# Performance work log

Measured on AMD Instinct MI355X. Metric: run time of the kernel, lower is better.

## Reference

```python
import jax, jax.numpy as jnp
import numpy as np
from jax import lax

EPS = 1e-07
B, NPRIM, NSEC, DP, DS = 512, 1152, 10, 8, 16


def setup_inputs() -> dict:
    key = jax.random.key(0)
    ks = jax.random.split(key, 12)
    inp = {}
    inp['x'] = jax.random.uniform(ks[0], (B, 28, 28, 1), dtype=jnp.float32)
    inp['labels'] = jax.random.randint(ks[1], (B,), 0, NSEC)
    # conv1: 9x9, 1 -> 256, relu ; conv2 (primary caps): 9x9 stride2, 256 -> 256
    inp['conv1_k'] = jax.random.normal(ks[2], (9, 9, 1, 256), dtype=jnp.float32) * 0.05
    inp['conv1_b'] = jnp.zeros((256,), dtype=jnp.float32)
    inp['conv2_k'] = jax.random.normal(ks[3], (9, 9, 256, 256), dtype=jnp.float32) * 0.02
    inp['conv2_b'] = jnp.zeros((256,), dtype=jnp.float32)
    # pose transform W: [1152, 10, 16, 8]
    inp['w'] = jax.random.normal(ks[4], (NPRIM, NSEC, DS, DP), dtype=jnp.float32) * 0.05
    # decoder
    inp['d1_w'] = jax.random.normal(ks[5], (NSEC * DS, 512), dtype=jnp.float32) * 0.05
    inp['d1_b'] = jnp.zeros((512,), dtype=jnp.float32)
    inp['d2_w'] = jax.random.normal(ks[6], (512, 1024), dtype=jnp.float32) * 0.05
    inp['d2_b'] = jnp.zeros((1024,), dtype=jnp.float32)
    inp['d3_w'] = jax.random.normal(ks[7], (1024, 784), dtype=jnp.float32) * 0.05
    inp['d3_b'] = jnp.zeros((784,), dtype=jnp.float32)
    return inp


def _conv(x, k, b, stride):
    y = lax.conv_general_dilated(x, k, (stride, stride), 'VALID',
                                 dimension_numbers=('NHWC', 'HWIO', 'NHWC'))
    return y + b


def _squash(s):
    # s: [..., D]
    s_norm = jnp.linalg.norm(s, axis=-1, keepdims=True)
    sq = jnp.square(s_norm)
    return sq / (1.0 + sq) * s / (s_norm + EPS)


def reference(x, labels, conv1_k, conv1_b, conv2_k, conv2_b, w,
              d1_w, d1_b, d2_w, d2_b, d3_w, d3_b):
    h = jax.nn.relu(_conv(x, conv1_k, conv1_b, 1))        # [B,20,20,256]
    p = _conv(h, conv2_k, conv2_b, 2)                      # [B,6,6,256]
    u = p.reshape(x.shape[0], NPRIM, DP)                   # [B,1152,8]
    # u_hat[b,n,s,d] = sum_p w[n,s,d,p] * u[b,n,p]
    u_hat = jnp.einsum('nsdp,bnp->bnsd', w, u)             # [B,1152,10,16]

    b_logits = jnp.zeros((x.shape[0], NPRIM, NSEC, 1), dtype=u_hat.dtype)
    v = None
    for _ in range(3):  # r routing iterations (fixed, small)
        c = jax.nn.softmax(b_logits, axis=-2)              # softmax over 10 secondary caps
        s = jnp.sum(c * u_hat, axis=1, keepdims=True)      # [B,1,10,16]
        v = _squash(s)                                     # [B,1,10,16]
        agreement = jnp.sum(u_hat * v, axis=-1, keepdims=True)  # [B,1152,10,1]
        b_logits = b_logits + agreement

    y = jax.nn.one_hot(labels, NSEC, dtype=v.dtype)        # [B,10]
    mask = y[:, None, :, None]                             # [B,1,10,1]
    v_masked = mask * v
    v_flat = v_masked.reshape(-1, NSEC * DS)               # [B,160]
    r1 = jax.nn.relu(v_flat @ d1_w + d1_b)
    r2 = jax.nn.relu(r1 @ d2_w + d2_b)
    recon = jax.nn.sigmoid(r2 @ d3_w + d3_b)               # [B,784]
    return v, recon
```

## Files before the change

### kernel.cpp

```cpp
#include <hip/hip_runtime.h>

#define USH unsigned short

__device__ inline float bf2f(USH u){ return __uint_as_float(((unsigned)u)<<16); }
__device__ inline USH f2bf(float f){
  unsigned u = __float_as_uint(f);
  return (USH)((u + 0x7FFFu + ((u>>16)&1u))>>16);
}

typedef __attribute__((ext_vector_type(8))) short bf16x8;
typedef __attribute__((ext_vector_type(4))) float f32x4;

__device__ inline void gll16(const USH* g, USH* l){
  __builtin_amdgcn_global_load_lds((const __attribute__((address_space(1))) void*)g,
                                   (__attribute__((address_space(3))) void*)l, 16, 0, 0);
}

__global__ __launch_bounds__(256) void im2col_k(
    const float* __restrict__ x, USH* __restrict__ xcol)
{
  int b = blockIdx.x, t = threadIdx.x;
  __shared__ float xs[784];
  for (int i = t; i < 784; i += 256) xs[i] = x[b*784 + i];
  __syncthreads();
  USH* dst = xcol + (size_t)b*38400;
  for (int idx = t; idx < 38400; idx += 256) {
    int sp = idx / 96, k = idx - sp*96;
    int y = sp / 20, xx = sp - y*20;
    USH v = 0;
    if (k < 81) {
      int dy = k / 9, dx = k - dy*9;
      v = f2bf(xs[(y+dy)*28 + xx + dx]);
    }
    dst[idx] = v;
  }
}

__global__ __launch_bounds__(256) void tr_k1(const float* __restrict__ k1, USH* __restrict__ k1T)
{
  int n = threadIdx.x;
  for (int k = 0; k < 96; ++k)
    k1T[n*96 + k] = (k < 81) ? f2bf(k1[k*256 + n]) : (USH)0;
}

__global__ __launch_bounds__(256) void gemm1(
    const USH* __restrict__ xcol, const USH* __restrict__ k1T,
    const float* __restrict__ b1, USH* __restrict__ h)
{
  int t = threadIdx.x;
  int m0 = blockIdx.x * 64;
  int lane = t & 63, wave = t >> 6;
  int wn = wave * 64;
  int fr = lane & 15, fq = lane >> 4;

  f32x4 acc[4][4];
#pragma unroll
  for (int i = 0; i < 4; ++i)
#pragma unroll
    for (int j = 0; j < 4; ++j)
#pragma unroll
      for (int r = 0; r < 4; ++r) acc[i][j][r] = 0.f;

#pragma unroll
  for (int kt = 0; kt < 3; ++kt) {
    int kc = kt*32 + fq*8;
    bf16x8 af[4], bg[4];
#pragma unroll
    for (int mf = 0; mf < 4; ++mf)
      af[mf] = *(const bf16x8*)&xcol[(size_t)(m0 + mf*16 + fr)*96 + kc];
#pragma unroll
    for (int nf = 0; nf < 4; ++nf)
      bg[nf] = *(const bf16x8*)&k1T[(size_t)(wn + nf*16 + fr)*96 + kc];
#pragma unroll
    for (int mf = 0; mf < 4; ++mf)
#pragma unroll
      for (int nf = 0; nf < 4; ++nf)
        acc[mf][nf] = __builtin_amdgcn_mfma_f32_16x16x32_bf16(af[mf], bg[nf], acc[mf][nf], 0,0,0);
  }

#pragma unroll
  for (int mf = 0; mf < 4; ++mf)
#pragma unroll
    for (int nf = 0; nf < 4; ++nf) {
      int n = wn + nf*16 + fr;
      float bias = b1[n];
#pragma unroll
      for (int r = 0; r < 4; ++r) {
        int m = m0 + mf*16 + fq*4 + r;
        float v = acc[mf][nf][r] + bias;
        h[(size_t)m*256 + n] = f2bf(v > 0.f ? v : 0.f);
      }
    }
}

__global__ __launch_bounds__(256) void tr_k2(const float* __restrict__ k2, USH* __restrict__ k2T)
{
  __shared__ float tile[32][33];
  int kb = blockIdx.x*32, nb = blockIdx.y*32;
  int tx = threadIdx.x & 31, ty = threadIdx.x >> 5;
#pragma unroll
  for (int r = 0; r < 4; ++r) {
    int k = kb + ty + r*8;
    tile[ty + r*8][tx] = k2[(size_t)k*256 + nb + tx];
  }
  __syncthreads();
#pragma unroll
  for (int r = 0; r < 4; ++r) {
    int n = nb + ty + r*8;
    k2T[(size_t)n*20736 + kb + tx] = f2bf(tile[tx][ty + r*8]);
  }
}

__global__ __launch_bounds__(256) void conv2_mfma(
    const USH* __restrict__ h, const USH* __restrict__ k2T,
    float* __restrict__ up)
{
  __shared__ __align__(16) USH Asm[2][128*64];
  __shared__ __align__(16) USH Bsm[2][64*64];
  int t = threadIdx.x;
  int mb = blockIdx.x, nb = blockIdx.y, ksl = blockIdx.z;

  int sg = (((t&7) ^ ((t>>3)&7)) << 3);

  int arow_off[4];
#pragma unroll
  for (int i = 0; i < 4; ++i) {
    int row = (t>>3) + i*32;
    int m = mb*128 + row;
    int bb = m/36, r = m - bb*36;
    int oy = r/6, ox = r - oy*6;
    arow_off[i] = bb*102400 + oy*10240 + ox*512 + sg;
  }
  int brow_off[2];
#pragma unroll
  for (int i = 0; i < 2; ++i) {
    int nl = (t>>3) + i*32;
    brow_off[i] = (nb*64 + nl)*20736 + sg;
  }

  int lane = t & 63;
  int wave = t >> 6;
  int wm = (wave>>1)*64, wn = (wave&1)*32;
  int fr = lane & 15, fq = lane >> 4;

  f32x4 acc[4][2];
#pragma unroll
  for (int i = 0; i < 4; ++i)
#pragma unroll
    for (int j = 0; j < 2; ++j)
#pragma unroll
      for (int r = 0; r < 4; ++r) acc[i][j][r] = 0.f;

  int rg0 = (((0*4 + fq) ^ (fr&7)) << 3);
  int rg1 = (((1*4 + fq) ^ (fr&7)) << 3);

#define STAGE(buf, kt) do {                                            \
    int j_ = (kt) >> 2;                                                \
    int cin0_ = ((kt) & 3) << 6;                                       \
    int dy_ = j_/9, dx_ = j_ - dy_*9;                                  \
    int koff_ = (dy_*20 + dx_)*256 + cin0_;                            \
    USH* Ad_ = &Asm[buf][(t>>6)*512];                                  \
    USH* Bd_ = &Bsm[buf][(t>>6)*512];                                  \
    _Pragma("unroll")                                                  \
    for (int i_ = 0; i_ < 4; ++i_) gll16(h + arow_off[i_] + koff_, Ad_ + i_*2048); \
    _Pragma("unroll")                                                  \
    for (int i_ = 0; i_ < 2; ++i_) gll16(k2T + brow_off[i_] + (kt)*64, Bd_ + i_*2048); \
  } while(0)

  const int k0 = ksl*81, kend = k0 + 81;
  STAGE(0, k0);
  __syncthreads();

  int cur = 0;
  for (int kt = k0; kt < kend; ++kt) {
    if (kt + 1 < kend) STAGE(cur^1, kt+1);

    bf16x8 af[4][2], bg[2][2];
#pragma unroll
    for (int mf = 0; mf < 4; ++mf) {
      af[mf][0] = *(const bf16x8*)&Asm[cur][(wm + mf*16 + fr)*64 + rg0];
      af[mf][1] = *(const bf16x8*)&Asm[cur][(wm + mf*16 + fr)*64 + rg1];
    }
#pragma unroll
    for (int nf = 0; nf < 2; ++nf) {
      bg[nf][0] = *(const bf16x8*)&Bsm[cur][(wn + nf*16 + fr)*64 + rg0];
      bg[nf][1] = *(const bf16x8*)&Bsm[cur][(wn + nf*16 + fr)*64 + rg1];
    }
#pragma unroll
    for (int mf = 0; mf < 4; ++mf)
#pragma unroll
      for (int nf = 0; nf < 2; ++nf) {
        acc[mf][nf] = __builtin_amdgcn_mfma_f32_16x16x32_bf16(af[mf][0], bg[nf][0], acc[mf][nf], 0,0,0);
        acc[mf][nf] = __builtin_amdgcn_mfma_f32_16x16x32_bf16(af[mf][1], bg[nf][1], acc[mf][nf], 0,0,0);
      }
    __syncthreads();
    cur ^= 1;
  }
#undef STAGE

  float* dst = up + (size_t)ksl*4718592;
#pragma unroll
  for (int mf = 0; mf < 4; ++mf)
#pragma unroll
    for (int nf = 0; nf < 2; ++nf) {
      int n = nb*64 + wn + nf*16 + fr;
#pragma unroll
      for (int r = 0; r < 4; ++r) {
        int m = mb*128 + wm + mf*16 + fq*4 + r;
        dst[(size_t)m*256 + n] = acc[mf][nf][r];
      }
    }
}

__global__ __launch_bounds__(256) void reduce_u(
    const float* __restrict__ up, const float* __restrict__ b2, float* __restrict__ u)
{
  int i = blockIdx.x*256 + threadIdx.x;
  f32x4 a = *(const f32x4*)&up[(size_t)i*4];
  f32x4 b = *(const f32x4*)&up[4718592ull + (size_t)i*4];
  f32x4 c = *(const f32x4*)&up[9437184ull + (size_t)i*4];
  f32x4 d = *(const f32x4*)&up[14155776ull + (size_t)i*4];
  int n0 = (i*4) & 255;
  f32x4 o;
#pragma unroll
  for (int j = 0; j < 4; ++j) o[j] = (a[j] + b[j]) + (c[j] + d[j]) + b2[n0 + j];
  *(f32x4*)&u[(size_t)i*4] = o;
}

__global__ __launch_bounds__(192) void wsum_tr(const float* __restrict__ w,
    float* __restrict__ Ws)
{
  int n = blockIdx.x, t = threadIdx.x;
  __shared__ float wn[1280];
  for (int i = t; i < 1280; i += 192) wn[i] = w[n*1280 + i];
  __syncthreads();
  if (t < 160) {
#pragma unroll
    for (int p = 0; p < 8; ++p)
      Ws[((size_t)n*8 + p)*160 + t] = wn[(t>>4)*128 + (t&15)*8 + p];
  }
}

__global__ __launch_bounds__(192) void p1gemm(const float* __restrict__ u,
    const float* __restrict__ Ws, float* __restrict__ part)
{
  int b0 = blockIdx.x*32, k0 = blockIdx.y*288;
  int t = threadIdx.x;
  __shared__ float usm[288*36];
  for (int i = t; i < 288*32; i += 192) {
    int bl = i/288, kk = i - bl*288;
    usm[kk*36 + bl] = u[(size_t)(b0+bl)*9216 + k0 + kk];
  }
  __syncthreads();
  if (t < 160) {
    const float* wp = Ws + (size_t)k0*160 + t;
#pragma unroll 1
    for (int half = 0; half < 2; ++half) {
      float acc[16];
#pragma unroll
      for (int i = 0; i < 16; ++i) acc[i] = 0.f;
      for (int kk = 0; kk < 288; ++kk) {
        float wv = wp[(size_t)kk*160];
        const f32x4* ub = (const f32x4*)&usm[kk*36 + half*16];
        f32x4 u0 = ub[0], u1 = ub[1], u2 = ub[2], u3 = ub[3];
#pragma unroll
        for (int i = 0; i < 4; ++i) {
          acc[i]    += u0[i]*wv;
          acc[4+i]  += u1[i]*wv;
          acc[8+i]  += u2[i]*wv;
          acc[12+i] += u3[i]*wv;
        }
      }
      float* pp = &part[((size_t)blockIdx.y*512 + b0 + half*16)*160 + t];
#pragma unroll
      for (int i = 0; i < 16; ++i) pp[(size_t)i*160] = acc[i];
    }
  }
}

__global__ __launch_bounds__(192) void squash1(const float* __restrict__ part,
    float* __restrict__ vout)
{
  int b = blockIdx.x, t = threadIdx.x;
  if (t < 160) {
    float sv = 0.f;
    for (int ks = 0; ks < 32; ++ks) sv += part[((size_t)ks*512 + b)*160 + t];
    sv *= 0.1f;
    float n2 = sv*sv;
    n2 += __shfl_xor(n2, 1, 16);
    n2 += __shfl_xor(n2, 2, 16);
    n2 += __shfl_xor(n2, 4, 16);
    n2 += __shfl_xor(n2, 8, 16);
    float nrm = sqrtf(n2);
    float o = (n2/(1.f + n2)) * sv / (nrm + 1e-7f);
    vout[b*160 + t] = o;
  }
}

__global__ __launch_bounds__(256) void uhat_kernel(
    const float* __restrict__ u, const float* __restrict__ w, USH* __restrict__ uh)
{
  int n = blockIdx.x, b0 = blockIdx.y*64;
  int t = threadIdx.x;
  __shared__ float wsm[20*65];
  __shared__ float usm[512];
  for (int i = t; i < 1280; i += 256) wsm[(i>>6)*65 + (i&63)] = w[n*1280 + i];
  for (int i = t; i < 512; i += 256) {
    int bl = i>>3, p = i&7;
    usm[i] = u[(size_t)(b0+bl)*9216 + n*8 + p];
  }
  __syncthreads();
  USH* dst = uh + ((size_t)n*512 + b0)*160;
  for (int v = t; v < 1280; v += 256) {
    int bl = v/20, oct = v - bl*20;
    const float* upt = &usm[bl*8];
    bf16x8 pk;
#pragma unroll
    for (int j = 0; j < 8; ++j) {
      const float* wp = &wsm[oct*65 + j*8];
      float a = 0.f;
#pragma unroll
      for (int p = 0; p < 8; ++p) a += wp[p]*upt[p];
      pk[j] = (short)f2bf(a);
    }
    *(bf16x8*)&dst[(size_t)v*8] = pk;
  }
}

template<int PASS>
__global__ __launch_bounds__(256) void route_part(
    const USH* __restrict__ uh, const float* __restrict__ vin,
    float* __restrict__ L, float* __restrict__ partR)
{
  int b = blockIdx.x, nc = blockIdx.y;
  int t = threadIdx.x;
  int lane = t & 63, w = t >> 6;
  int grp = lane >> 4, s = lane & 15;
  int stream = w*4 + grp;
  bool act = s < 10;

  float vr[16];
  {
    const float* vp = vin + b*160 + s*16;
#pragma unroll
    for (int d = 0; d < 16; ++d) vr[d] = act ? vp[d] : 0.f;
  }
  float acc[16];
#pragma unroll
  for (int d = 0; d < 16; ++d) acc[d] = 0.f;

  int nbase = nc*288 + stream*18;
  for (int ni = 0; ni < 18; ++ni) {
    int n = nbase + ni;
    float uv[16];
    if (act) {
      const USH* upt = uh + ((size_t)n*512 + b)*160 + s*16;
      bf16x8 p0 = *(const bf16x8*)upt;
      bf16x8 p1 = *(const bf16x8*)(upt + 8);
#pragma unroll
      for (int d = 0; d < 8; ++d) { uv[d] = bf2f((USH)p0[d]); uv[8+d] = bf2f((USH)p1[d]); }
    } else {
#pragma unroll
      for (int d = 0; d < 16; ++d) uv[d] = 0.f;
    }

    float dot = 0.f;
#pragma unroll
    for (int d = 0; d < 16; ++d) dot += uv[d]*vr[d];
    float lg;
    if (PASS == 2) {
      lg = dot;
      if (act) L[((size_t)n*512 + b)*10 + s] = dot;
    } else {
      lg = act ? (L[((size_t)n*512 + b)*10 + s] + dot) : 0.f;
    }
    if (!act) lg = -1e30f;
    float mx = lg;
    mx = fmaxf(mx, __shfl_xor(mx, 1, 16));
    mx = fmaxf(mx, __shfl_xor(mx, 2, 16));
    mx = fmaxf(mx, __shfl_xor(mx, 4, 16));
    mx = fmaxf(mx, __shfl_xor(mx, 8, 16));
    float e = __expf(lg - mx);
    float sum = e;
    sum += __shfl_xor(sum, 1, 16);
    sum += __shfl_xor(sum, 2, 16);
    sum += __shfl_xor(sum, 4, 16);
    sum += __shfl_xor(sum, 8, 16);
    float c = e / sum;
#pragma unroll
    for (int d = 0; d < 16; ++d) acc[d] += c*uv[d];
  }

  __shared__ float red[16][168];
  if (act) {
#pragma unroll
    for (int d = 0; d < 16; ++d) red[stream][s*16 + d] = acc[d];
  }
  __syncthreads();
  if (t < 160) {
    float sv = 0.f;
#pragma unroll
    for (int k = 0; k < 16; ++k) sv += red[k][t];
    partR[((size_t)nc*512 + b)*160 + t] = sv;
  }
}

template<int PASS>
__global__ __launch_bounds__(192) void squash_part(const float* __restrict__ partR,
    float* __restrict__ vout, float* __restrict__ vext)
{
  int b = blockIdx.x, t = threadIdx.x;
  if (t < 160) {
    float sv = 0.f;
#pragma unroll
    for (int nc = 0; nc < 4; ++nc) sv += partR[((size_t)nc*512 + b)*160 + t];
    float n2 = sv*sv;
    n2 += __shfl_xor(n2, 1, 16);
    n2 += __shfl_xor(n2, 2, 16);
    n2 += __shfl_xor(n2, 4, 16);
    n2 += __shfl_xor(n2, 8, 16);
    float nrm = sqrtf(n2);
    float o = (n2/(1.f + n2)) * sv / (nrm + 1e-7f);
    vout[b*160 + t] = o;
    if (PASS == 3) vext[b*160 + t] = o;
  }
}

__global__ __launch_bounds__(512) void d1_kernel(const float* __restrict__ v3,
    const int* __restrict__ labels, const float* __restrict__ w,
    const float* __restrict__ bias, float* __restrict__ r1)
{
  int b = blockIdx.x; int j = threadIdx.x;
  int lb = labels[b];
  float acc = bias[j];
#pragma unroll
  for (int d = 0; d < 16; ++d)
    acc += v3[b*160 + lb*16 + d] * w[(lb*16 + d)*512 + j];
  r1[(size_t)b*512 + j] = acc > 0.f ? acc : 0.f;
}

__global__ __launch_bounds__(256) void d2_kernel(const float* __restrict__ a,
    const float* __restrict__ w, const float* __restrict__ bias, float* __restrict__ o)
{
  int j = blockIdx.x*256 + threadIdx.x;
  int b0 = blockIdx.y*4;
  __shared__ float as[4*512];
  for (int i = threadIdx.x; i < 4*512; i += 256) as[i] = a[(size_t)(b0 + (i>>9))*512 + (i&511)];
  __syncthreads();
  float acc[4];
  float bs = bias[j];
#pragma unroll
  for (int i = 0; i < 4; ++i) acc[i] = bs;
  for (int k = 0; k < 512; ++k) {
    float wv = w[(size_t)k*1024 + j];
#pragma unroll
    for (int i = 0; i < 4; ++i) acc[i] += as[i*512 + k]*wv;
  }
#pragma unroll
  for (int i = 0; i < 4; ++i)
    o[(size_t)(b0+i)*1024 + j] = acc[i] > 0.f ? acc[i] : 0.f;
}

__global__ __launch_bounds__(256) void d3_kernel(const float* __restrict__ a,
    const float* __restrict__ w, const float* __restrict__ bias, float* __restrict__ o)
{
  int j = blockIdx.x*256 + threadIdx.x;
  int b0 = blockIdx.y*4;
  __shared__ float as[4*1024];
  for (int i = threadIdx.x; i < 4*1024; i += 256) as[i] = a[(size_t)(b0 + (i>>10))*1024 + (i&1023)];
  __syncthreads();
  if (j < 784) {
    float acc[4];
    float bs = bias[j];
#pragma unroll
    for (int i = 0; i < 4; ++i) acc[i] = bs;
    for (int k = 0; k < 1024; ++k) {
      float wv = w[(size_t)k*784 + j];
#pragma unroll
      for (int i = 0; i < 4; ++i) acc[i] += as[i*1024 + k]*wv;
    }
#pragma unroll
    for (int i = 0; i < 4; ++i)
      o[(size_t)(b0+i)*784 + j] = 1.f/(1.f + __expf(-acc[i]));
  }
}

extern "C" void kernel_launch(void* const* d_in, const int* in_sizes, int n_in,
                              void* d_out, int out_size, void* d_ws, size_t ws_size,
                              hipStream_t stream)
{
  const float* x   = (const float*)d_in[0];
  const int*   lab = (const int*)  d_in[1];
  const float* k1  = (const float*)d_in[2];
  const float* b1  = (const float*)d_in[3];
  const float* k2  = (const float*)d_in[4];
  const float* b2  = (const float*)d_in[5];
  const float* w   = (const float*)d_in[6];
  const float* d1w = (const float*)d_in[7];
  const float* d1b = (const float*)d_in[8];
  const float* d2w = (const float*)d_in[9];
  const float* d2b = (const float*)d_in[10];
  const float* d3w = (const float*)d_in[11];
  const float* d3b = (const float*)d_in[12];
  float* out = (float*)d_out;

  char* ws = (char*)d_ws;
  USH*   uh    = (USH*)(ws + 0);
  USH*   h     = (USH*)(ws + 0);
  float* up    = (float*)(ws + 104857600ull);
  USH*   xcol  = (USH*)(ws + 142606336ull);
  float* u     = (float*)(ws + 188743680ull);
  USH*   k2T   = (USH*)(ws + 207618048ull);
  float* part  = (float*)(ws + 207618048ull);
  float* partR = (float*)(ws + 207618048ull);
  float* L     = (float*)(ws + 218234880ull);
  float* Wsum  = (float*)(ws + 218234880ull);
  USH*   k1T   = (USH*)(ws + 241827840ull);
  float* v1    = (float*)(ws + 242155520ull);
  float* v2    = (float*)(ws + 242483200ull);
  float* v3    = (float*)(ws + 242810880ull);
  float* r1    = (float*)(ws + 243138560ull);
  float* r2    = (float*)(ws + 244187136ull);

  im2col_k<<<512, 256, 0, stream>>>(x, xcol);
  tr_k1<<<1, 256, 0, stream>>>(k1, k1T);
  gemm1<<<3200, 256, 0, stream>>>(xcol, k1T, b1, h);

  tr_k2<<<dim3(648,8), 256, 0, stream>>>(k2, k2T);
  conv2_mfma<<<dim3(144,4,4), 256, 0, stream>>>(h, k2T, up);
  reduce_u<<<4608, 256, 0, stream>>>(up, b2, u);

  wsum_tr<<<1152, 192, 0, stream>>>(w, Wsum);
  p1gemm<<<dim3(16,32), 192, 0, stream>>>(u, Wsum, part);
  squash1<<<512, 192, 0, stream>>>(part, v1);

  uhat_kernel<<<dim3(1152,8), 256, 0, stream>>>(u, w, uh);

  route_part<2><<<dim3(512,4), 256, 0, stream>>>(uh, v1, L, partR);
  squash_part<2><<<512, 192, 0, stream>>>(partR, v2, nullptr);
  route_part<3><<<dim3(512,4), 256, 0, stream>>>(uh, v2, L, partR);
  squash_part<3><<<512, 192, 0, stream>>>(partR, v3, out);

  d1_kernel<<<512, 512, 0, stream>>>(v3, lab, d1w, d1b, r1);
  d2_kernel<<<dim3(4,128), 256, 0, stream>>>(r1, d2w, d2b, r2);
  d3_kernel<<<dim3(4,128), 256, 0, stream>>>(r2, d3w, d3b, out + 81920);
}
```

Baseline: 689.1 us.

## Fuse u_hat computation into routing passes instead of materializing bf16 u_hat

Removes the separate uhat kernel that wrote a ~189MB bf16 u_hat tensor and instead recomputes u_hat on the fly inside each routing pass from u and W staged in LDS with double-buffered W tiles. Blocks are retiled to 16 primary capsules by 16 batch elements, giving 72 partial sums that the squash kernel now reduces. This trades the large global write and two full reads for extra FMAs and per-iteration barriers, and it also computes u_hat in fp32 rather than bf16.

Measured after the change: 731.5 us. 1.06x slower.

```diff
diff --git a/kernel.cpp b/kernel.cpp
--- a/kernel.cpp
+++ b/kernel.cpp
@@ -297,84 +297,75 @@
   }
 }
 
-__global__ __launch_bounds__(256) void uhat_kernel(
-    const float* __restrict__ u, const float* __restrict__ w, USH* __restrict__ uh)
-{
-  int n = blockIdx.x, b0 = blockIdx.y*64;
+template<int PASS>
+__global__ __launch_bounds__(256) void route_ns(
+    const float* __restrict__ u, const float* __restrict__ w,
+    const float* __restrict__ vin, float* __restrict__ L,
+    float* __restrict__ partR)
+{
+  int ng = blockIdx.x, bc = blockIdx.y;
+  int n0 = ng*16, b0 = bc*16;
   int t = threadIdx.x;
-  __shared__ float wsm[20*65];
-  __shared__ float usm[512];
-  for (int i = t; i < 1280; i += 256) wsm[(i>>6)*65 + (i&63)] = w[n*1280 + i];
-  for (int i = t; i < 512; i += 256) {
-    int bl = i>>3, p = i&7;
-    usm[i] = u[(size_t)(b0+bl)*9216 + n*8 + p];
-  }
-  __syncthreads();
-  USH* dst = uh + ((size_t)n*512 + b0)*160;
-  for (int v = t; v < 1280; v += 256) {
-    int bl = v/20, oct = v - bl*20;
-    const float* upt = &usm[bl*8];
-    bf16x8 pk;
-#pragma unroll
-    for (int j = 0; j < 8; ++j) {
-      const float* wp = &wsm[oct*65 + j*8];
-      float a = 0.f;
-#pragma unroll
-      for (int p = 0; p < 8; ++p) a += wp[p]*upt[p];
-      pk[j] = (short)f2bf(a);
-    }
-    *(bf16x8*)&dst[(size_t)v*8] = pk;
-  }
-}
-
-template<int PASS>
-__global__ __launch_bounds__(256) void route_part(
-    const USH* __restrict__ uh, const float* __restrict__ vin,
-    float* __restrict__ L, float* __restrict__ partR)
-{
-  int b = blockIdx.x, nc = blockIdx.y;
-  int t = threadIdx.x;
-  int lane = t & 63, w = t >> 6;
-  int grp = lane >> 4, s = lane & 15;
-  int stream = w*4 + grp;
+  int lane = t & 63;
+  int s = lane & 15;
+  int bl = (t >> 6)*4 + (lane >> 4);
   bool act = s < 10;
+  int sw = act ? s : 0;
+  int b = b0 + bl;
+
+  __shared__ float u_lds[16][132];
+  __shared__ __align__(16) float wsm[2][20*68];
+
+  for (int i = t; i < 16*128; i += 256) {
+    int b_ = i >> 7, off = i & 127;
+    u_lds[b_][off] = u[(size_t)(b0+b_)*9216 + n0*8 + off];
+  }
+  for (int i = t; i < 1280; i += 256)
+    wsm[0][(i>>6)*68 + (i&63)] = w[(size_t)n0*1280 + i];
 
   float vr[16];
   {
-    const float* vp = vin + b*160 + s*16;
-#pragma unroll
-    for (int d = 0; d < 16; ++d) vr[d] = act ? vp[d] : 0.f;
+    const float* vp = vin + (size_t)b*160 + sw*16;
+#pragma unroll
+    for (int d = 0; d < 16; ++d) vr[d] = vp[d];
   }
   float acc[16];
 #pragma unroll
   for (int d = 0; d < 16; ++d) acc[d] = 0.f;
 
-  int nbase = nc*288 + stream*18;
-  for (int ni = 0; ni < 18; ++ni) {
-    int n = nbase + ni;
-    float uv[16];
-    if (act) {
-      const USH* upt = uh + ((size_t)n*512 + b)*160 + s*16;
-      bf16x8 p0 = *(const bf16x8*)upt;
-      bf16x8 p1 = *(const bf16x8*)(upt + 8);
-#pragma unroll
-      for (int d = 0; d < 8; ++d) { uv[d] = bf2f((USH)p0[d]); uv[8+d] = bf2f((USH)p1[d]); }
-    } else {
-#pragma unroll
-      for (int d = 0; d < 16; ++d) uv[d] = 0.f;
+  __syncthreads();
+
+  int cur = 0;
+  for (int ni = 0; ni < 16; ++ni) {
+    int n = n0 + ni;
+    if (ni + 1 < 16)
+      for (int i = t; i < 1280; i += 256)
+        wsm[cur^1][(i>>6)*68 + (i&63)] = w[(size_t)(n+1)*1280 + i];
+
+    f32x4 u0 = *(const f32x4*)&u_lds[bl][ni*8];
+    f32x4 u1 = *(const f32x4*)&u_lds[bl][ni*8 + 4];
+
+    float uh[16];
+#pragma unroll
+    for (int d = 0; d < 16; ++d) {
+      const float* wr = &wsm[cur][(2*sw + (d>>3))*68 + (d&7)*8];
+      f32x4 wa = *(const f32x4*)wr;
+      f32x4 wb = *(const f32x4*)(wr + 4);
+      uh[d] = wa[0]*u0[0]+wa[1]*u0[1]+wa[2]*u0[2]+wa[3]*u0[3]
+            + wb[0]*u1[0]+wb[1]*u1[1]+wb[2]*u1[2]+wb[3]*u1[3];
     }
 
     float dot = 0.f;
 #pragma unroll
-    for (int d = 0; d < 16; ++d) dot += uv[d]*vr[d];
+    for (int d = 0; d < 16; ++d) dot += uh[d]*vr[d];
+
     float lg;
     if (PASS == 2) {
-      lg = dot;
+      lg = act ? dot : -1e30f;
       if (act) L[((size_t)n*512 + b)*10 + s] = dot;
     } else {
-      lg = act ? (L[((size_t)n*512 + b)*10 + s] + dot) : 0.f;
-    }
-    if (!act) lg = -1e30f;
+      lg = act ? (dot + L[((size_t)n*512 + b)*10 + s]) : -1e30f;
+    }
     float mx = lg;
     mx = fmaxf(mx, __shfl_xor(mx, 1, 16));
     mx = fmaxf(mx, __shfl_xor(mx, 2, 16));
@@ -388,32 +379,32 @@
     sum += __shfl_xor(sum, 8, 16);
     float c = e / sum;
 #pragma unroll
-    for (int d = 0; d < 16; ++d) acc[d] += c*uv[d];
-  }
-
-  __shared__ float red[16][168];
+    for (int d = 0; d < 16; ++d) acc[d] += c*uh[d];
+
+    __syncthreads();
+    cur ^= 1;
+  }
+
   if (act) {
-#pragma unroll
-    for (int d = 0; d < 16; ++d) red[stream][s*16 + d] = acc[d];
-  }
-  __syncthreads();
-  if (t < 160) {
-    float sv = 0.f;
-#pragma unroll
-    for (int k = 0; k < 16; ++k) sv += red[k][t];
-    partR[((size_t)nc*512 + b)*160 + t] = sv;
+    float* pp = &partR[((size_t)ng*512 + b)*160 + s*16];
+#pragma unroll
+    for (int q = 0; q < 4; ++q) {
+      f32x4 o;
+#pragma unroll
+      for (int j = 0; j < 4; ++j) o[j] = acc[q*4 + j];
+      *(f32x4*)(pp + q*4) = o;
+    }
   }
 }
 
 template<int PASS>
-__global__ __launch_bounds__(192) void squash_part(const float* __restrict__ partR,
+__global__ __launch_bounds__(192) void squash72(const float* __restrict__ partR,
     float* __restrict__ vout, float* __restrict__ vext)
 {
   int b = blockIdx.x, t = threadIdx.x;
   if (t < 160) {
     float sv = 0.f;
-#pragma unroll
-    for (int nc = 0; nc < 4; ++nc) sv += partR[((size_t)nc*512 + b)*160 + t];
+    for (int g = 0; g < 72; ++g) sv += partR[((size_t)g*512 + b)*160 + t];
     float n2 = sv*sv;
     n2 += __shfl_xor(n2, 1, 16);
     n2 += __shfl_xor(n2, 2, 16);
@@ -505,14 +496,13 @@
   float* out = (float*)d_out;
 
   char* ws = (char*)d_ws;
-  USH*   uh    = (USH*)(ws + 0);
   USH*   h     = (USH*)(ws + 0);
+  float* partR = (float*)(ws + 0);
   float* up    = (float*)(ws + 104857600ull);
   USH*   xcol  = (USH*)(ws + 142606336ull);
   float* u     = (float*)(ws + 188743680ull);
   USH*   k2T   = (USH*)(ws + 207618048ull);
   float* part  = (float*)(ws + 207618048ull);
-  float* partR = (float*)(ws + 207618048ull);
   float* L     = (float*)(ws + 218234880ull);
   float* Wsum  = (float*)(ws + 218234880ull);
   USH*   k1T   = (USH*)(ws + 241827840ull);
@@ -534,12 +524,10 @@
   p1gemm<<<dim3(16,32), 192, 0, stream>>>(u, Wsum, part);
   squash1<<<512, 192, 0, stream>>>(part, v1);
 
-  uhat_kernel<<<dim3(1152,8), 256, 0, stream>>>(u, w, uh);
-
-  route_part<2><<<dim3(512,4), 256, 0, stream>>>(uh, v1, L, partR);
-  squash_part<2><<<512, 192, 0, stream>>>(partR, v2, nullptr);
-  route_part<3><<<dim3(512,4), 256, 0, stream>>>(uh, v2, L, partR);
-  squash_part<3><<<512, 192, 0, stream>>>(partR, v3, out);
+  route_ns<2><<<dim3(72,32), 256, 0, stream>>>(u, w, v1, L, partR);
+  squash72<2><<<512, 192, 0, stream>>>(partR, v2, nullptr);
+  route_ns<3><<<dim3(72,32), 256, 0, stream>>>(u, w, v2, L, partR);
+  squash72<3><<<512, 192, 0, stream>>>(partR, v3, out);
 
   d1_kernel<<<512, 512, 0, stream>>>(v3, lab, d1w, d1b, r1);
   d2_kernel<<<dim3(4,128), 256, 0, stream>>>(r1, d2w, d2b, r2);
```

## Replace stored routing logits with summed v vectors, prefetch u_hat, remap conv2 grid by XCD

Applied to the files above, without the earlier changes.

Routing pass 3 no longer reads logits stored in pass 2. Because agreement is linear in v, the logits equal the dot of u_hat with (v1+v2), so squash pass 2 writes that sum and route_part recomputes the logits from it. This removes the write and re-read of the [1152,512,10] logit buffer. The route loop also prefetches the next u_hat row into registers, and conv2 now uses a flat grid mapped so each XCD handles a contiguous range of M-tiles for better L2 reuse. The summed-v form changes floating-point rounding slightly compared with accumulating the logits step by step.

After: 618.6 us. 1.11x faster.

```diff
diff --git a/kernel.cpp b/kernel.cpp
--- a/kernel.cpp
+++ b/kernel.cpp
@@ -118,7 +118,14 @@
   __shared__ __align__(16) USH Asm[2][128*64];
   __shared__ __align__(16) USH Bsm[2][64*64];
   int t = threadIdx.x;
-  int mb = blockIdx.x, nb = blockIdx.y, ksl = blockIdx.z;
+  int flat = blockIdx.x;
+  int xcd  = flat & 7;
+  int slot = flat >> 3;
+  int nb   = slot & 3;
+  int rest = slot >> 2;
+  int mb_l = rest % 18;
+  int ksl  = rest / 18;
+  int mb   = xcd*18 + mb_l;
 
   int sg = (((t&7) ^ ((t>>3)&7)) << 3);
 
@@ -327,10 +334,9 @@
   }
 }
 
-template<int PASS>
 __global__ __launch_bounds__(256) void route_part(
     const USH* __restrict__ uh, const float* __restrict__ vin,
-    float* __restrict__ L, float* __restrict__ partR)
+    float* __restrict__ partR)
 {
   int b = blockIdx.x, nc = blockIdx.y;
   int t = threadIdx.x;
@@ -350,31 +356,33 @@
   for (int d = 0; d < 16; ++d) acc[d] = 0.f;
 
   int nbase = nc*288 + stream*18;
+  const USH* base = uh + ((size_t)nbase*512 + b)*160 + s*16;
+  const size_t nstride = (size_t)512*160;
+
+  bf16x8 c0{}, c1{};
+  if (act) { c0 = *(const bf16x8*)base; c1 = *(const bf16x8*)(base + 8); }
+
   for (int ni = 0; ni < 18; ++ni) {
-    int n = nbase + ni;
+    bf16x8 f0 = c0, f1 = c1;
+    if (ni + 1 < 18 && act) {
+      const USH* p = base + (size_t)(ni+1)*nstride;
+      f0 = *(const bf16x8*)p;
+      f1 = *(const bf16x8*)(p + 8);
+    }
     float uv[16];
     if (act) {
-      const USH* upt = uh + ((size_t)n*512 + b)*160 + s*16;
-      bf16x8 p0 = *(const bf16x8*)upt;
-      bf16x8 p1 = *(const bf16x8*)(upt + 8);
-#pragma unroll
-      for (int d = 0; d < 8; ++d) { uv[d] = bf2f((USH)p0[d]); uv[8+d] = bf2f((USH)p1[d]); }
+#pragma unroll
+      for (int d = 0; d < 8; ++d) { uv[d] = bf2f((USH)c0[d]); uv[8+d] = bf2f((USH)c1[d]); }
     } else {
 #pragma unroll
       for (int d = 0; d < 16; ++d) uv[d] = 0.f;
     }
+    c0 = f0; c1 = f1;
 
     float dot = 0.f;
 #pragma unroll
     for (int d = 0; d < 16; ++d) dot += uv[d]*vr[d];
-    float lg;
-    if (PASS == 2) {
-      lg = dot;
-      if (act) L[((size_t)n*512 + b)*10 + s] = dot;
-    } else {
-      lg = act ? (L[((size_t)n*512 + b)*10 + s] + dot) : 0.f;
-    }
-    if (!act) lg = -1e30f;
+    float lg = act ? dot : -1e30f;
     float mx = lg;
     mx = fmaxf(mx, __shfl_xor(mx, 1, 16));
     mx = fmaxf(mx, __shfl_xor(mx, 2, 16));
@@ -407,7 +415,7 @@
 
 template<int PASS>
 __global__ __launch_bounds__(192) void squash_part(const float* __restrict__ partR,
-    float* __restrict__ vout, float* __restrict__ vext)
+    const float* __restrict__ vprev, float* __restrict__ vout, float* __restrict__ vext)
 {
   int b = blockIdx.x, t = threadIdx.x;
   if (t < 160) {
@@ -422,6 +430,7 @@
     float nrm = sqrtf(n2);
     float o = (n2/(1.f + n2)) * sv / (nrm + 1e-7f);
     vout[b*160 + t] = o;
+    if (PASS == 2) vext[b*160 + t] = vprev[b*160 + t] + o;
     if (PASS == 3) vext[b*160 + t] = o;
   }
 }
@@ -513,21 +522,21 @@
   USH*   k2T   = (USH*)(ws + 207618048ull);
   float* part  = (float*)(ws + 207618048ull);
   float* partR = (float*)(ws + 207618048ull);
-  float* L     = (float*)(ws + 218234880ull);
   float* Wsum  = (float*)(ws + 218234880ull);
   USH*   k1T   = (USH*)(ws + 241827840ull);
   float* v1    = (float*)(ws + 242155520ull);
   float* v2    = (float*)(ws + 242483200ull);
   float* v3    = (float*)(ws + 242810880ull);
-  float* r1    = (float*)(ws + 243138560ull);
-  float* r2    = (float*)(ws + 244187136ull);
+  float* vsum  = (float*)(ws + 243138560ull);
+  float* r1    = (float*)(ws + 243466240ull);
+  float* r2    = (float*)(ws + 244514816ull);
 
   im2col_k<<<512, 256, 0, stream>>>(x, xcol);
   tr_k1<<<1, 256, 0, stream>>>(k1, k1T);
   gemm1<<<3200, 256, 0, stream>>>(xcol, k1T, b1, h);
 
   tr_k2<<<dim3(648,8), 256, 0, stream>>>(k2, k2T);
-  conv2_mfma<<<dim3(144,4,4), 256, 0, stream>>>(h, k2T, up);
+  conv2_mfma<<<2304, 256, 0, stream>>>(h, k2T, up);
   reduce_u<<<4608, 256, 0, stream>>>(up, b2, u);
 
   wsum_tr<<<1152, 192, 0, stream>>>(w, Wsum);
@@ -536,10 +545,10 @@
 
   uhat_kernel<<<dim3(1152,8), 256, 0, stream>>>(u, w, uh);
 
-  route_part<2><<<dim3(512,4), 256, 0, stream>>>(uh, v1, L, partR);
-  squash_part<2><<<512, 192, 0, stream>>>(partR, v2, nullptr);
-  route_part<3><<<dim3(512,4), 256, 0, stream>>>(uh, v2, L, partR);
-  squash_part<3><<<512, 192, 0, stream>>>(partR, v3, out);
+  route_part<<<dim3(512,4), 256, 0, stream>>>(uh, v1, partR);
+  squash_part<2><<<512, 192, 0, stream>>>(partR, v1, v2, vsum);
+  route_part<<<dim3(512,4), 256, 0, stream>>>(uh, vsum, partR);
+  squash_part<3><<<512, 192, 0, stream>>>(partR, nullptr, v3, out);
 
   d1_kernel<<<512, 512, 0, stream>>>(v3, lab, d1w, d1b, r1);
   d2_kernel<<<dim3(4,128), 256, 0, stream>>>(r1, d2w, d2b, r2);
```
